# Optimization experiments

Hardware: AMD Instinct MI355X
Metric: run time of the kernel (lower is better)

## Reference

```python
import jax, jax.numpy as jnp
import numpy as np

B, LQ, LKV, D, H = 4, 1024, 2048, 1024, 16
HD = D // H
EPS = 1e-5
NEG = -1e9


def _layernorm(x, w, b):
    mu = jnp.mean(x, axis=-1, keepdims=True)
    var = jnp.mean(jnp.square(x - mu), axis=-1, keepdims=True)
    return (x - mu) * jax.lax.rsqrt(var + EPS) * w + b


def setup_inputs() -> dict:
    key = jax.random.key(0)
    ks = jax.random.split(key, 10)
    q = jax.random.normal(ks[0], (B, LQ, D), dtype=jnp.float32)
    kv = jax.random.normal(ks[1], (B, LKV, D), dtype=jnp.float32)
    # ragged kv lengths; mask True == padding
    lengths = jax.random.randint(ks[2], (B,), LKV // 4, LKV + 1)
    mask = jnp.arange(LKV)[None, :] >= lengths[:, None]  # [B, LKV] bool
    s = 1.0 / np.sqrt(D)
    params = dict(
        norm_q_w=jnp.ones((D,), jnp.float32),
        norm_q_b=jnp.zeros((D,), jnp.float32),
        norm_kv_w=jnp.ones((D,), jnp.float32),
        norm_kv_b=jnp.zeros((D,), jnp.float32),
        Wq=jax.random.normal(ks[3], (D, D), jnp.float32) * s,
        bq=jnp.zeros((D,), jnp.float32),
        Wkv=jax.random.normal(ks[4], (2 * D, D), jnp.float32) * s,
        bkv=jnp.zeros((2 * D,), jnp.float32),
        Wo=jax.random.normal(ks[5], (D, D), jnp.float32) * s,
        bo=jnp.zeros((D,), jnp.float32),
    )
    return dict(q=q, kv=kv, mask=mask, **params)


def reference(q, kv, mask, norm_q_w, norm_q_b, norm_kv_w, norm_kv_b, Wq, bq, Wkv, bkv, Wo, bo):
    q_res = q
    qn = _layernorm(q, norm_q_w, norm_q_b)
    kvn = _layernorm(kv, norm_kv_w, norm_kv_b)
    # projections
    qh = (qn @ Wq.T + bq).reshape(B, LQ, H, HD)
    kvp = (kvn @ Wkv.T + bkv).reshape(B, LKV, 2, H, HD)
    k, v = kvp[:, :, 0], kvp[:, :, 1]  # [B, LKV, H, HD]
    # masked cross attention (math-equivalent to varlen flash attn over unpadded kv)
    scale = 1.0 / np.sqrt(HD)
    scores = jnp.einsum('bqhd,bkhd->bhqk', qh, k) * scale
    scores = jnp.where(mask[:, None, None, :], NEG, scores)
    attn = jax.nn.softmax(scores, axis=-1)
    out = jnp.einsum('bhqk,bkhd->bqhd', attn, v).reshape(B, LQ, D)
    # out proj + residual (dropout is identity in eval)
    return q_res + (out @ Wo.T + bo)


if __name__ == '__main__':
    inp = setup_inputs()
    y = reference(**inp)
    print(y.shape, y.dtype)
```

## Files before the change

### kernel.cpp

```cpp
#include <hip/hip_runtime.h>

#define DEV __device__ __forceinline__

typedef unsigned short u16;
typedef float  floatx4 __attribute__((ext_vector_type(4)));
typedef unsigned int uintx4 __attribute__((ext_vector_type(4)));
typedef __bf16 bf16x8 __attribute__((ext_vector_type(8)));

constexpr int cB = 4, cLQ = 1024, cLKV = 2048, cD = 1024, cH = 16, cHD = 64;

DEV u16 f2bf(float f) {
  unsigned u = __builtin_bit_cast(unsigned, f);
  u += 0x7fffu + ((u >> 16) & 1u);
  return (u16)(u >> 16);
}

DEV u16 f2bf_t(float f) {
  return (u16)(__builtin_bit_cast(unsigned, f) >> 16);
}

DEV bf16x8 ld_frag(const u16* p) {
  uintx4 u = *(const uintx4*)p;
  return __builtin_bit_cast(bf16x8, u);
}

DEV floatx4 mfma16(bf16x8 a, bf16x8 b, floatx4 c) {
  return __builtin_amdgcn_mfma_f32_16x16x32_bf16(a, b, c, 0, 0, 0);
}

DEV float ex2(float x) { return __builtin_amdgcn_exp2f(x); }

__global__ __launch_bounds__(256) void prep_kernel(
    const float* __restrict__ q, const float* __restrict__ kv,
    const float* __restrict__ nqw, const float* __restrict__ nqb,
    const float* __restrict__ nkw, const float* __restrict__ nkb,
    u16* __restrict__ qn, u16* __restrict__ kvn,
    const float* __restrict__ Wq, const float* __restrict__ Wkv,
    const float* __restrict__ Wo, u16* __restrict__ wqb,
    u16* __restrict__ wkvb, u16* __restrict__ wob,
    const void* __restrict__ mask, int* __restrict__ lens) {
  int bid = blockIdx.x, tid = threadIdx.x;
  if (bid < cB * (cLQ + cLKV)) {
    const float* x; const float* w; const float* b; u16* dst;
    if (bid < cB * cLQ) {
      x = q + (size_t)bid * cD; w = nqw; b = nqb; dst = qn + (size_t)bid * cD;
    } else {
      int r2 = bid - cB * cLQ;
      x = kv + (size_t)r2 * cD; w = nkw; b = nkb; dst = kvn + (size_t)r2 * cD;
    }
    float4 v = ((const float4*)x)[tid];
    __shared__ float sbuf[8];
    float s = v.x + v.y + v.z + v.w;
    #pragma unroll
    for (int m = 1; m < 64; m <<= 1) s += __shfl_xor(s, m, 64);
    if ((tid & 63) == 0) sbuf[tid >> 6] = s;
    __syncthreads();
    float mean = (sbuf[0] + sbuf[1] + sbuf[2] + sbuf[3]) * (1.f / cD);
    float dx = v.x - mean, dy = v.y - mean, dz = v.z - mean, dw = v.w - mean;
    float ss = dx * dx + dy * dy + dz * dz + dw * dw;
    #pragma unroll
    for (int m = 1; m < 64; m <<= 1) ss += __shfl_xor(ss, m, 64);
    if ((tid & 63) == 0) sbuf[4 + (tid >> 6)] = ss;
    __syncthreads();
    float var = (sbuf[4] + sbuf[5] + sbuf[6] + sbuf[7]) * (1.f / cD);
    float rs = rsqrtf(var + 1e-5f);
    float4 wv = ((const float4*)w)[tid];
    float4 bv = ((const float4*)b)[tid];
    ushort4 o;
    o.x = f2bf(dx * rs * wv.x + bv.x);
    o.y = f2bf(dy * rs * wv.y + bv.y);
    o.z = f2bf(dz * rs * wv.z + bv.z);
    o.w = f2bf(dw * rs * wv.w + bv.w);
    ((ushort4*)dst)[tid] = o;
  } else if (bid < cB * (cLQ + cLKV) + 4096) {
    int gi = (bid - cB * (cLQ + cLKV)) * 256 + tid;
    const float* src; u16* dst; int off;
    if (gi < 262144)      { src = Wq;  dst = wqb;  off = gi; }
    else if (gi < 786432) { src = Wkv; dst = wkvb; off = gi - 262144; }
    else                  { src = Wo;  dst = wob;  off = gi - 786432; }
    float4 v = ((const float4*)src)[off];
    ushort4 o;
    o.x = f2bf(v.x); o.y = f2bf(v.y); o.z = f2bf(v.z); o.w = f2bf(v.w);
    ((ushort4*)dst)[off] = o;
  } else {
    __shared__ int smode;
    __shared__ int cnt[cB];
    if (tid == 0) smode = 0;
    if (tid < cB) cnt[tid] = 0;
    __syncthreads();
    const unsigned* mi = (const unsigned*)mask;
    int bad = 0;
    for (int i = tid; i < cB * cLKV / 4; i += 256)
      if (mi[i] > 1u) bad = 1;
    if (bad) smode = 1;
    __syncthreads();
    if (smode == 0) {
      for (int b = 0; b < cB; b++) {
        int c = 0;
        for (int i = tid; i < cLKV; i += 256) c += (mi[(size_t)b * cLKV + i] == 0u);
        atomicAdd(&cnt[b], c);
      }
    } else {
      const unsigned char* m8 = (const unsigned char*)mask;
      for (int b = 0; b < cB; b++) {
        int c = 0;
        for (int i = tid; i < cLKV; i += 256) c += (m8[(size_t)b * cLKV + i] == 0);
        atomicAdd(&cnt[b], c);
      }
    }
    __syncthreads();
    if (tid < cB) lens[tid] = cnt[tid];
  }
}

struct TileCtx {
  int m16, quad, wr, wc;
};

DEV void gemm_mainloop(const u16* __restrict__ A, const u16* __restrict__ Bm,
                       int row0, int col0, int K, u16* As, u16* Bs,
                       const TileCtx& t, floatx4 (&acc)[4][4]) {
  int tid = threadIdx.x;
  int wave = tid >> 6, lane = tid & 63;
  int srow = wave * 16 + (lane >> 2);
  int sseg = (lane & 3) * 8;
  const u16* ga = A + (size_t)(row0 + srow) * K + sseg;
  const u16* gb = Bm + (size_t)(col0 + srow) * K + sseg;
  const size_t rstep = (size_t)64 * K;
  int woff = srow * 32 + sseg;

  uintx4 a0 = *(const uintx4*)ga;
  uintx4 a1 = *(const uintx4*)(ga + rstep);
  uintx4 b0 = *(const uintx4*)gb;
  uintx4 b1 = *(const uintx4*)(gb + rstep);
  *(uintx4*)(As + woff) = a0;
  *(uintx4*)(As + woff + 2048) = a1;
  *(uintx4*)(Bs + woff) = b0;
  *(uintx4*)(Bs + woff + 2048) = b1;
  a0 = *(const uintx4*)(ga + 32);
  a1 = *(const uintx4*)(ga + rstep + 32);
  b0 = *(const uintx4*)(gb + 32);
  b1 = *(const uintx4*)(gb + rstep + 32);
  __syncthreads();

  for (int k0 = 0; k0 < K; k0 += 32) {
    int cur = (k0 >> 5) & 1;
    const u16* rA = As + cur * 4096;
    const u16* rB = Bs + cur * 4096;
    bf16x8 af[4], bfr[4];
    #pragma unroll
    for (int i = 0; i < 4; i++)
      af[i] = ld_frag(&rA[(t.wr * 64 + i * 16 + t.m16) * 32 + t.quad * 8]);
    #pragma unroll
    for (int j = 0; j < 4; j++)
      bfr[j] = ld_frag(&rB[(t.wc * 64 + j * 16 + t.m16) * 32 + t.quad * 8]);
    if (k0 + 32 < K) {
      u16* nA = As + (cur ^ 1) * 4096 + woff;
      u16* nB = Bs + (cur ^ 1) * 4096 + woff;
      *(uintx4*)nA = a0;
      *(uintx4*)(nA + 2048) = a1;
      *(uintx4*)nB = b0;
      *(uintx4*)(nB + 2048) = b1;
      if (k0 + 64 < K) {
        a0 = *(const uintx4*)(ga + k0 + 64);
        a1 = *(const uintx4*)(ga + rstep + k0 + 64);
        b0 = *(const uintx4*)(gb + k0 + 64);
        b1 = *(const uintx4*)(gb + rstep + k0 + 64);
      }
    }
    #pragma unroll
    for (int i = 0; i < 4; i++)
      #pragma unroll
      for (int j = 0; j < 4; j++)
        acc[i][j] = mfma16(af[i], bfr[j], acc[i][j]);
    __syncthreads();
  }
}

__global__ __launch_bounds__(256) void proj_fused(
    const u16* __restrict__ qn, const u16* __restrict__ wqb,
    const float* __restrict__ bq, u16* __restrict__ qhb,
    const u16* __restrict__ kvn, const u16* __restrict__ wkvb,
    const float* __restrict__ bkv, u16* __restrict__ khb,
    u16* __restrict__ vthb) {
  __shared__ __align__(16) u16 As[2 * 128 * 32];
  __shared__ __align__(16) u16 Bs[2 * 128 * 32];
  int bid = blockIdx.x;
  int lane = threadIdx.x & 63;
  TileCtx t;
  t.m16 = lane & 15; t.quad = lane >> 4;
  int wave = threadIdx.x >> 6;
  t.wr = wave >> 1; t.wc = wave & 1;

  bool isQ = bid < 256;
  int row0, col0;
  const u16* A; const u16* Bm; const float* bias;
  if (isQ) {
    row0 = (bid >> 3) * 128; col0 = (bid & 7) * 128;
    A = qn; Bm = wqb; bias = bq;
  } else {
    int b2 = bid - 256;
    row0 = (b2 >> 4) * 128; col0 = (b2 & 15) * 128;
    A = kvn; Bm = wkvb; bias = bkv;
  }

  floatx4 z = {0.f, 0.f, 0.f, 0.f};
  floatx4 acc[4][4];
  #pragma unroll
  for (int i = 0; i < 4; i++)
    #pragma unroll
    for (int j = 0; j < 4; j++) acc[i][j] = z;

  gemm_mainloop(A, Bm, row0, col0, cD, As, Bs, t, acc);

  #pragma unroll
  for (int j = 0; j < 4; j++) {
    int col = col0 + t.wc * 64 + j * 16 + t.m16;
    float bs = bias[col];
    if (isQ) {
      #pragma unroll
      for (int i = 0; i < 4; i++) {
        int crow = row0 + t.wr * 64 + i * 16 + t.quad * 4;
        #pragma unroll
        for (int r = 0; r < 4; r++)
          qhb[(size_t)(crow + r) * cD + col] =
              f2bf((acc[i][j][r] + bs) * 0.18033688f);
      }
    } else {
      bool isK = col < cD;
      int c2 = isK ? col : col - cD;
      int hh = c2 >> 6, dd = c2 & 63;
      #pragma unroll
      for (int i = 0; i < 4; i++) {
        int crow = row0 + t.wr * 64 + i * 16 + t.quad * 4;
        int bb = crow >> 11, kvp = crow & (cLKV - 1);
        if (isK) {
          u16* dst = khb + ((size_t)(bb * cH + hh) * cLKV + kvp) * 64 + dd;
          #pragma unroll
          for (int r = 0; r < 4; r++) dst[(size_t)r * 64] = f2bf(acc[i][j][r] + bs);
        } else {
          u16* dst = vthb + ((size_t)(bb * cH + hh) * 64 + dd) * cLKV + kvp;
          ushort4 o;
          o.x = f2bf(acc[i][j][0] + bs);
          o.y = f2bf(acc[i][j][1] + bs);
          o.z = f2bf(acc[i][j][2] + bs);
          o.w = f2bf(acc[i][j][3] + bs);
          *(ushort4*)dst = o;
        }
      }
    }
  }
}

__global__ __launch_bounds__(256) void gemm_o(
    const u16* __restrict__ A, const u16* __restrict__ Bm,
    const float* __restrict__ bias, const float* __restrict__ res,
    float* __restrict__ Cout, int N, int K) {
  __shared__ __align__(16) u16 As[2 * 128 * 32];
  __shared__ __align__(16) u16 Bs[2 * 128 * 32];
  int lane = threadIdx.x & 63;
  TileCtx t;
  t.m16 = lane & 15; t.quad = lane >> 4;
  int wave = threadIdx.x >> 6;
  t.wr = wave >> 1; t.wc = wave & 1;
  int row0 = blockIdx.y * 128, col0 = blockIdx.x * 128;

  floatx4 z = {0.f, 0.f, 0.f, 0.f};
  floatx4 acc[4][4];
  #pragma unroll
  for (int i = 0; i < 4; i++)
    #pragma unroll
    for (int j = 0; j < 4; j++) acc[i][j] = z;

  gemm_mainloop(A, Bm, row0, col0, K, As, Bs, t, acc);

  #pragma unroll
  for (int j = 0; j < 4; j++) {
    int col = col0 + t.wc * 64 + j * 16 + t.m16;
    float bs = bias[col];
    #pragma unroll
    for (int i = 0; i < 4; i++) {
      int crow = row0 + t.wr * 64 + i * 16 + t.quad * 4;
      #pragma unroll
      for (int r = 0; r < 4; r++) {
        size_t idx = (size_t)(crow + r) * N + col;
        Cout[idx] = acc[i][j][r] + bs + res[idx];
      }
    }
  }
}

constexpr int PS = 72;

template<bool MASK>
DEV void attn_tile(int k0, int len, const u16* __restrict__ kg,
                   const u16* __restrict__ vg, u16* __restrict__ psw,
                   const bf16x8 (&qf)[2][2], int m16, int quad,
                   float (&lsum)[2], floatx4 (&accO)[2][4]) {
  floatx4 z = {0.f, 0.f, 0.f, 0.f};
  uintx4 kld[4][2];
  #pragma unroll
  for (int t = 0; t < 4; t++) {
    const u16* kp = kg + (size_t)(k0 + t * 16) * cHD;
    kld[t][0] = *(const uintx4*)kp;
    kld[t][1] = *(const uintx4*)(kp + 32);
  }
  uintx4 vld[2][4];
  #pragma unroll
  for (int ks = 0; ks < 2; ks++)
    #pragma unroll
    for (int db = 0; db < 4; db++)
      vld[ks][db] = *(const uintx4*)(vg + (size_t)(db * 16) * cLKV + k0 + ks * 32);

  floatx4 s[2][4];
  #pragma unroll
  for (int g = 0; g < 2; g++)
    #pragma unroll
    for (int t = 0; t < 4; t++) {
      floatx4 tt = z;
      tt = mfma16(__builtin_bit_cast(bf16x8, kld[t][0]), qf[g][0], tt);
      tt = mfma16(__builtin_bit_cast(bf16x8, kld[t][1]), qf[g][1], tt);
      s[g][t] = tt;
    }

  #pragma unroll
  for (int g = 0; g < 2; g++) {
    #pragma unroll
    for (int t = 0; t < 4; t++) {
      float e0, e1, e2, e3;
      if (MASK) {
        int key = k0 + t * 16 + quad * 4;
        e0 = (key     < len) ? ex2(s[g][t][0]) : 0.f;
        e1 = (key + 1 < len) ? ex2(s[g][t][1]) : 0.f;
        e2 = (key + 2 < len) ? ex2(s[g][t][2]) : 0.f;
        e3 = (key + 3 < len) ? ex2(s[g][t][3]) : 0.f;
      } else {
        e0 = ex2(s[g][t][0]);
        e1 = ex2(s[g][t][1]);
        e2 = ex2(s[g][t][2]);
        e3 = ex2(s[g][t][3]);
      }
      lsum[g] += (e0 + e1) + (e2 + e3);
      ushort4 pk;
      pk.x = f2bf_t(e0); pk.y = f2bf_t(e1); pk.z = f2bf_t(e2); pk.w = f2bf_t(e3);
      *(ushort4*)&psw[(g * 16 + m16) * PS + t * 16 + quad * 4] = pk;
    }
  }

  #pragma unroll
  for (int g = 0; g < 2; g++) {
    bf16x8 ap0 = ld_frag(&psw[(g * 16 + m16) * PS + quad * 8]);
    bf16x8 ap1 = ld_frag(&psw[(g * 16 + m16) * PS + 32 + quad * 8]);
    #pragma unroll
    for (int db = 0; db < 4; db++) {
      accO[g][db] = mfma16(ap0, __builtin_bit_cast(bf16x8, vld[0][db]), accO[g][db]);
      accO[g][db] = mfma16(ap1, __builtin_bit_cast(bf16x8, vld[1][db]), accO[g][db]);
    }
  }
}

__global__ __launch_bounds__(256) void attn_kernel(
    const u16* __restrict__ qh, const u16* __restrict__ kh,
    const u16* __restrict__ vth, const int* __restrict__ lens,
    u16* __restrict__ out) {
  int bid = blockIdx.x;
  int i = bid >> 3;
  int h = (bid & 7) * 2 + (i & 1);
  int b = ((i >> 1) & 1) | (((i >> 5) & 1) << 1);
  int qb = (i >> 2) & 7;
  int len = lens[b];
  int wave = threadIdx.x >> 6, lane = threadIdx.x & 63;
  int m16 = lane & 15, quad = lane >> 4;

  __shared__ __align__(16) u16 Ps[4][32 * PS];
  u16* psw = &Ps[wave][0];

  int q0 = qb * 128 + wave * 32;
  const u16* qp = qh + ((size_t)(b * cLQ + q0 + m16) * cH + h) * cHD;
  bf16x8 qf[2][2];
  qf[0][0] = ld_frag(qp + quad * 8);
  qf[0][1] = ld_frag(qp + 32 + quad * 8);
  qf[1][0] = ld_frag(qp + (size_t)16 * cD + quad * 8);
  qf[1][1] = ld_frag(qp + (size_t)16 * cD + 32 + quad * 8);

  const u16* kg = kh + (size_t)(b * cH + h) * cLKV * cHD
                     + (size_t)m16 * cHD + quad * 8;
  const u16* vg = vth + (size_t)(b * cH + h) * cHD * cLKV
                      + (size_t)m16 * cLKV + quad * 8;

  float lsum[2] = {0.f, 0.f};
  floatx4 z = {0.f, 0.f, 0.f, 0.f};
  floatx4 accO[2][4] = {{z, z, z, z}, {z, z, z, z}};

  int nfull = len >> 6;
  for (int c = 0; c < nfull; c++)
    attn_tile<false>(c * 64, len, kg, vg, psw, qf, m16, quad, lsum, accO);
  if (len & 63)
    attn_tile<true>(nfull * 64, len, kg, vg, psw, qf, m16, quad, lsum, accO);

  #pragma unroll
  for (int g = 0; g < 2; g++) {
    float tsum = lsum[g];
    tsum += __shfl_xor(tsum, 16, 64);
    tsum += __shfl_xor(tsum, 32, 64);
    #pragma unroll
    for (int r = 0; r < 4; r++) {
      float inv = 1.0f / __shfl(tsum, quad * 4 + r, 16);
      int qg = q0 + g * 16 + quad * 4 + r;
      size_t base = ((size_t)(b * cLQ + qg) * cH + h) * cHD;
      #pragma unroll
      for (int db = 0; db < 4; db++)
        out[base + db * 16 + m16] = f2bf(accO[g][db][r] * inv);
    }
  }
}

extern "C" void kernel_launch(void* const* d_in, const int* in_sizes, int n_in,
                              void* d_out, int out_size, void* d_ws, size_t ws_size,
                              hipStream_t stream) {
  const float* q    = (const float*)d_in[0];
  const float* kv   = (const float*)d_in[1];
  const void*  mask = d_in[2];
  const float* nqw  = (const float*)d_in[3];
  const float* nqb  = (const float*)d_in[4];
  const float* nkw  = (const float*)d_in[5];
  const float* nkb  = (const float*)d_in[6];
  const float* Wq   = (const float*)d_in[7];
  const float* bq   = (const float*)d_in[8];
  const float* Wkv  = (const float*)d_in[9];
  const float* bkv  = (const float*)d_in[10];
  const float* Wo   = (const float*)d_in[11];
  const float* bo   = (const float*)d_in[12];
  float* out = (float*)d_out;

  char* w = (char*)d_ws;
  int* lens = (int*)w;       w += 256;
  u16* qn   = (u16*)w;       w += (size_t)cB * cLQ * cD * 2;
  u16* kvn  = (u16*)w;       w += (size_t)cB * cLKV * cD * 2;
  u16* wqb  = (u16*)w;       w += (size_t)cD * cD * 2;
  u16* wkvb = (u16*)w;       w += (size_t)2 * cD * cD * 2;
  u16* wob  = (u16*)w;       w += (size_t)cD * cD * 2;
  u16* qhb  = (u16*)w;       w += (size_t)cB * cLQ * cD * 2;
  u16* khb  = (u16*)w;       w += (size_t)cB * cH * cLKV * cHD * 2;
  u16* vthb = (u16*)w;       w += (size_t)cB * cH * cHD * cLKV * 2;
  u16* aob  = (u16*)w;

  prep_kernel<<<cB * (cLQ + cLKV) + 4096 + 1, 256, 0, stream>>>(
      q, kv, nqw, nqb, nkw, nkb, qn, kvn,
      Wq, Wkv, Wo, wqb, wkvb, wob, mask, lens);
  proj_fused<<<1280, 256, 0, stream>>>(
      qn, wqb, bq, qhb, kvn, wkvb, bkv, khb, vthb);
  attn_kernel<<<512, 256, 0, stream>>>(
      qhb, khb, vthb, lens, aob);
  gemm_o<<<dim3(cD / 128, cB * cLQ / 128), 256, 0, stream>>>(
      aob, wob, bo, q, out, cD, cD);
}
```

Before: 312.0 us.

## Share K/V tiles via LDS in attention, length-sort batches, swizzle GEMM block order

The attention kernel now stages each 64-key K and V tile cooperatively into shared memory with register prefetch of the next tile. All four waves reuse the tile instead of each wave loading K/V from global memory separately. The prep kernel sorts batches by kv length, and attention blocks are scheduled longest-batch first to balance ragged work. Both projection GEMM and output GEMM get block-index swizzles for better L2/XCD locality. The cost is extra barriers per tile and added LDS use, which may lower occupancy.

```diff
diff --git a/kernel.cpp b/kernel.cpp
--- a/kernel.cpp
+++ b/kernel.cpp
@@ -110,6 +110,18 @@
     }
     __syncthreads();
     if (tid < cB) lens[tid] = cnt[tid];
+    if (tid == 0) {
+      int ord[4] = {0, 1, 2, 3};
+      #pragma unroll
+      for (int a = 0; a < 3; a++)
+        #pragma unroll
+        for (int d = 0; d < 3; d++)
+          if (cnt[ord[d]] < cnt[ord[d + 1]]) {
+            int tswap = ord[d]; ord[d] = ord[d + 1]; ord[d + 1] = tswap;
+          }
+      #pragma unroll
+      for (int a = 0; a < 4; a++) lens[4 + a] = ord[a];
+    }
   }
 }
 
@@ -185,7 +197,8 @@
     u16* __restrict__ vthb) {
   __shared__ __align__(16) u16 As[2 * 128 * 32];
   __shared__ __align__(16) u16 Bs[2 * 128 * 32];
-  int bid = blockIdx.x;
+  int bid0 = blockIdx.x;
+  int bid = (bid0 & 7) * 160 + (bid0 >> 3);
   int lane = threadIdx.x & 63;
   TileCtx t;
   t.m16 = lane & 15; t.quad = lane >> 4;
@@ -258,12 +271,14 @@
     float* __restrict__ Cout, int N, int K) {
   __shared__ __align__(16) u16 As[2 * 128 * 32];
   __shared__ __align__(16) u16 Bs[2 * 128 * 32];
+  int bid0 = blockIdx.x;
+  int swz = (bid0 & 7) * 32 + (bid0 >> 3);
+  int row0 = (swz >> 3) * 128, col0 = (swz & 7) * 128;
   int lane = threadIdx.x & 63;
   TileCtx t;
   t.m16 = lane & 15; t.quad = lane >> 4;
   int wave = threadIdx.x >> 6;
   t.wr = wave >> 1; t.wc = wave & 1;
-  int row0 = blockIdx.y * 128, col0 = blockIdx.x * 128;
 
   floatx4 z = {0.f, 0.f, 0.f, 0.f};
   floatx4 acc[4][4];
@@ -290,41 +305,33 @@
   }
 }
 
+constexpr int KS = 72;
 constexpr int PS = 72;
 
 template<bool MASK>
-DEV void attn_tile(int k0, int len, const u16* __restrict__ kg,
-                   const u16* __restrict__ vg, u16* __restrict__ psw,
-                   const bf16x8 (&qf)[2][2], int m16, int quad,
-                   float (&lsum)[2], floatx4 (&accO)[2][4]) {
+DEV void attn_compute(int k0, int len, const u16* __restrict__ Kt,
+                      const u16* __restrict__ Vt, u16* __restrict__ psw,
+                      const bf16x8 (&qf)[2][2], int m16, int quad,
+                      float (&lsum)[2], floatx4 (&accO)[2][4]) {
   floatx4 z = {0.f, 0.f, 0.f, 0.f};
-  uintx4 kld[4][2];
+  bf16x8 kf[4][2];
   #pragma unroll
   for (int t = 0; t < 4; t++) {
-    const u16* kp = kg + (size_t)(k0 + t * 16) * cHD;
-    kld[t][0] = *(const uintx4*)kp;
-    kld[t][1] = *(const uintx4*)(kp + 32);
-  }
-  uintx4 vld[2][4];
-  #pragma unroll
-  for (int ks = 0; ks < 2; ks++)
-    #pragma unroll
-    for (int db = 0; db < 4; db++)
-      vld[ks][db] = *(const uintx4*)(vg + (size_t)(db * 16) * cLKV + k0 + ks * 32);
-
+    kf[t][0] = ld_frag(&Kt[(t * 16 + m16) * KS + quad * 8]);
+    kf[t][1] = ld_frag(&Kt[(t * 16 + m16) * KS + 32 + quad * 8]);
+  }
   floatx4 s[2][4];
   #pragma unroll
   for (int g = 0; g < 2; g++)
     #pragma unroll
     for (int t = 0; t < 4; t++) {
       floatx4 tt = z;
-      tt = mfma16(__builtin_bit_cast(bf16x8, kld[t][0]), qf[g][0], tt);
-      tt = mfma16(__builtin_bit_cast(bf16x8, kld[t][1]), qf[g][1], tt);
+      tt = mfma16(kf[t][0], qf[g][0], tt);
+      tt = mfma16(kf[t][1], qf[g][1], tt);
       s[g][t] = tt;
     }
-
-  #pragma unroll
-  for (int g = 0; g < 2; g++) {
+  #pragma unroll
+  for (int g = 0; g < 2; g++)
     #pragma unroll
     for (int t = 0; t < 4; t++) {
       float e0, e1, e2, e3;
@@ -345,16 +352,20 @@
       pk.x = f2bf_t(e0); pk.y = f2bf_t(e1); pk.z = f2bf_t(e2); pk.w = f2bf_t(e3);
       *(ushort4*)&psw[(g * 16 + m16) * PS + t * 16 + quad * 4] = pk;
     }
-  }
-
+  bf16x8 ap0[2], ap1[2];
   #pragma unroll
   for (int g = 0; g < 2; g++) {
-    bf16x8 ap0 = ld_frag(&psw[(g * 16 + m16) * PS + quad * 8]);
-    bf16x8 ap1 = ld_frag(&psw[(g * 16 + m16) * PS + 32 + quad * 8]);
-    #pragma unroll
-    for (int db = 0; db < 4; db++) {
-      accO[g][db] = mfma16(ap0, __builtin_bit_cast(bf16x8, vld[0][db]), accO[g][db]);
-      accO[g][db] = mfma16(ap1, __builtin_bit_cast(bf16x8, vld[1][db]), accO[g][db]);
+    ap0[g] = ld_frag(&psw[(g * 16 + m16) * PS + quad * 8]);
+    ap1[g] = ld_frag(&psw[(g * 16 + m16) * PS + 32 + quad * 8]);
+  }
+  #pragma unroll
+  for (int db = 0; db < 4; db++) {
+    bf16x8 bv0 = ld_frag(&Vt[(db * 16 + m16) * KS + quad * 8]);
+    bf16x8 bv1 = ld_frag(&Vt[(db * 16 + m16) * KS + 32 + quad * 8]);
+    #pragma unroll
+    for (int g = 0; g < 2; g++) {
+      accO[g][db] = mfma16(ap0[g], bv0, accO[g][db]);
+      accO[g][db] = mfma16(ap1[g], bv1, accO[g][db]);
     }
   }
 }
@@ -364,18 +375,22 @@
     const u16* __restrict__ vth, const int* __restrict__ lens,
     u16* __restrict__ out) {
   int bid = blockIdx.x;
-  int i = bid >> 3;
-  int h = (bid & 7) * 2 + (i & 1);
-  int b = ((i >> 1) & 1) | (((i >> 5) & 1) << 1);
-  int qb = (i >> 2) & 7;
+  int r = bid >> 7;
+  int rank = r ^ (r >> 1);
+  int b = lens[4 + rank];
+  int combo = bid & 127;
+  int h = combo >> 3;
+  int qt = combo & 7;
   int len = lens[b];
   int wave = threadIdx.x >> 6, lane = threadIdx.x & 63;
   int m16 = lane & 15, quad = lane >> 4;
 
+  __shared__ __align__(16) u16 Kt[64 * KS];
+  __shared__ __align__(16) u16 Vt[64 * KS];
   __shared__ __align__(16) u16 Ps[4][32 * PS];
   u16* psw = &Ps[wave][0];
 
-  int q0 = qb * 128 + wave * 32;
+  int q0 = qt * 128 + wave * 32;
   const u16* qp = qh + ((size_t)(b * cLQ + q0 + m16) * cH + h) * cHD;
   bf16x8 qf[2][2];
   qf[0][0] = ld_frag(qp + quad * 8);
@@ -383,20 +398,44 @@
   qf[1][0] = ld_frag(qp + (size_t)16 * cD + quad * 8);
   qf[1][1] = ld_frag(qp + (size_t)16 * cD + 32 + quad * 8);
 
-  const u16* kg = kh + (size_t)(b * cH + h) * cLKV * cHD
-                     + (size_t)m16 * cHD + quad * 8;
-  const u16* vg = vth + (size_t)(b * cH + h) * cHD * cLKV
-                      + (size_t)m16 * cLKV + quad * 8;
+  const u16* kbase = kh + (size_t)(b * cH + h) * cLKV * cHD;
+  const u16* vbase = vth + (size_t)(b * cH + h) * cHD * cLKV;
+
+  int srow = threadIdx.x >> 3;
+  int sseg = threadIdx.x & 7;
+  const u16* kg = kbase + (size_t)srow * cHD + sseg * 8;
+  const u16* vg = vbase + (size_t)srow * cLKV + sseg * 8;
 
   float lsum[2] = {0.f, 0.f};
   floatx4 z = {0.f, 0.f, 0.f, 0.f};
   floatx4 accO[2][4] = {{z, z, z, z}, {z, z, z, z}};
 
-  int nfull = len >> 6;
-  for (int c = 0; c < nfull; c++)
-    attn_tile<false>(c * 64, len, kg, vg, psw, qf, m16, quad, lsum, accO);
-  if (len & 63)
-    attn_tile<true>(nfull * 64, len, kg, vg, psw, qf, m16, quad, lsum, accO);
+  int nch = (len + 63) >> 6;
+  uintx4 ka  = *(const uintx4*)kg;
+  uintx4 kb2 = *(const uintx4*)(kg + (size_t)32 * cHD);
+  uintx4 va  = *(const uintx4*)vg;
+  uintx4 vb  = *(const uintx4*)(vg + (size_t)32 * cLKV);
+
+  for (int c = 0; c < nch; c++) {
+    int k0 = c * 64;
+    __syncthreads();
+    *(uintx4*)&Kt[srow * KS + sseg * 8] = ka;
+    *(uintx4*)&Kt[(srow + 32) * KS + sseg * 8] = kb2;
+    *(uintx4*)&Vt[srow * KS + sseg * 8] = va;
+    *(uintx4*)&Vt[(srow + 32) * KS + sseg * 8] = vb;
+    if (c + 1 < nch) {
+      int kn = k0 + 64;
+      ka  = *(const uintx4*)(kg + (size_t)kn * cHD);
+      kb2 = *(const uintx4*)(kg + (size_t)(kn + 32) * cHD);
+      va  = *(const uintx4*)(vg + kn);
+      vb  = *(const uintx4*)(vg + (size_t)32 * cLKV + kn);
+    }
+    __syncthreads();
+    if (k0 + 64 <= len)
+      attn_compute<false>(k0, len, Kt, Vt, psw, qf, m16, quad, lsum, accO);
+    else
+      attn_compute<true>(k0, len, Kt, Vt, psw, qf, m16, quad, lsum, accO);
+  }
 
   #pragma unroll
   for (int g = 0; g < 2; g++) {
@@ -404,13 +443,13 @@
     tsum += __shfl_xor(tsum, 16, 64);
     tsum += __shfl_xor(tsum, 32, 64);
     #pragma unroll
-    for (int r = 0; r < 4; r++) {
-      float inv = 1.0f / __shfl(tsum, quad * 4 + r, 16);
-      int qg = q0 + g * 16 + quad * 4 + r;
+    for (int rr = 0; rr < 4; rr++) {
+      float inv = 1.0f / __shfl(tsum, quad * 4 + rr, 16);
+      int qg = q0 + g * 16 + quad * 4 + rr;
       size_t base = ((size_t)(b * cLQ + qg) * cH + h) * cHD;
       #pragma unroll
       for (int db = 0; db < 4; db++)
-        out[base + db * 16 + m16] = f2bf(accO[g][db][r] * inv);
+        out[base + db * 16 + m16] = f2bf(accO[g][db][rr] * inv);
     }
   }
 }
@@ -452,6 +491,6 @@
       qn, wqb, bq, qhb, kvn, wkvb, bkv, khb, vthb);
   attn_kernel<<<512, 256, 0, stream>>>(
       qhb, khb, vthb, lens, aob);
-  gemm_o<<<dim3(cD / 128, cB * cLQ / 128), 256, 0, stream>>>(
+  gemm_o<<<dim3(256), 256, 0, stream>>>(
       aob, wob, bo, q, out, cD, cD);
 }
```

New measurement: 262.0 us. 16.0% less time.
